# Kernel optimization log

Hardware: AMD Instinct MI355X
Metric: run time of the kernel (lower is better)

## Reference

```python
import jax, jax.numpy as jnp
import numpy as np

N_NODES = 100000
N_EDGES = 1600000
D_IN, D_H, D_OUT = 128, 64, 32


def _linear_init(key, out_dim, in_dim):
    # torch.nn.Linear default init: U(-1/sqrt(in), 1/sqrt(in))
    bound = 1.0 / np.sqrt(in_dim)
    return jax.random.uniform(key, (out_dim, in_dim), jnp.float32, -bound, bound)


def setup_inputs() -> dict:
    key = jax.random.key(0)
    ks = jax.random.split(key, 8)
    x = jax.random.normal(ks[0], (N_NODES, D_IN), dtype=jnp.float32)
    edge_index = jax.random.randint(ks[1], (2, N_EDGES), 0, N_NODES, dtype=jnp.int64)
    return {
        "x": x,
        "edge_index": edge_index,
        # SAGEConv layer 1: lin_l (neighbor agg, with bias), lin_r (root, no bias)
        "W1_l": _linear_init(ks[2], D_H, D_IN),
        "b1": jnp.zeros((D_H,), jnp.float32),
        "W1_r": _linear_init(ks[3], D_H, D_IN),
        # SAGEConv layer 2
        "W2_l": _linear_init(ks[4], D_OUT, D_H),
        "b2": jnp.zeros((D_OUT,), jnp.float32),
        "W2_r": _linear_init(ks[5], D_OUT, D_H),
    }


def _sage_conv(x, src, dst, W_l, b_l, W_r):
    """PyG SAGEConv with mean aggregation: lin_l(mean_{j in N(i)} x_j) + lin_r(x_i)."""
    n = x.shape[0]
    # scatter-mean of source features onto destination nodes
    agg = jax.ops.segment_sum(x[src], dst, num_segments=n)          # [N, d]
    deg = jax.ops.segment_sum(jnp.ones_like(dst, dtype=x.dtype), dst, num_segments=n)
    mean = agg / jnp.maximum(deg, 1.0)[:, None]
    return mean @ W_l.T + b_l + x @ W_r.T


def reference(x, edge_index, W1_l, b1, W1_r, W2_l, b2, W2_r):
    src, dst = edge_index[0], edge_index[1]
    h = _sage_conv(x, src, dst, W1_l, b1, W1_r)
    h = jax.nn.relu(h)
    # dropout p=0.5 is identity in eval mode
    return _sage_conv(h, src, dst, W2_l, b2, W2_r)
```

## Files before the change

kernel.cpp:

```cpp
#include <hip/hip_runtime.h>


namespace {
constexpr int N = 100000;
constexpr int E = 1600000;
constexpr int NBLK = (N + 255) / 256;
constexpr int NT16 = N / 16;
constexpr int NCHUNK = 64;
constexpr int CHUNK_N = 1600;
constexpr int CAP = 28000;
constexpr int PA_BLOCKS = 256;
constexpr int PER_BLK = E / PA_BLOCKS;
}

using bf16x8 = __attribute__((ext_vector_type(8))) short;
using f32x4  = __attribute__((ext_vector_type(4))) float;

__device__ __forceinline__ short f2bf(float f) {
    unsigned u = __builtin_bit_cast(unsigned, f);
    u += 0x7FFFu + ((u >> 16) & 1u);
    return (short)(u >> 16);
}

__device__ __forceinline__ bf16x8 load_frag8(const float* __restrict__ p) {
    const float4* p4 = (const float4*)p;
    float4 f0 = p4[0], f1 = p4[1];
    bf16x8 r;
    r[0] = f2bf(f0.x); r[1] = f2bf(f0.y); r[2] = f2bf(f0.z); r[3] = f2bf(f0.w);
    r[4] = f2bf(f1.x); r[5] = f2bf(f1.y); r[6] = f2bf(f1.z); r[7] = f2bf(f1.w);
    return r;
}

__device__ __forceinline__ float pk_lo(unsigned u) {
    return __builtin_bit_cast(float, u << 16);
}
__device__ __forceinline__ float pk_hi(unsigned u) {
    return __builtin_bit_cast(float, u & 0xFFFF0000u);
}


__global__ __launch_bounds__(256) void detect_dtype(const int* __restrict__ raw,
                                                    int* __restrict__ flag,
                                                    int* __restrict__ bcur) {
    if (threadIdx.x < NCHUNK) bcur[threadIdx.x] = 0;
    int any = 0;
#pragma unroll
    for (int k = 0; k < 64; ++k) {
        int i = threadIdx.x + k * 256;
        any |= raw[2 * i + 1];
    }
    unsigned long long b = __ballot(any != 0);
    __shared__ int acc[4];
    int w = threadIdx.x >> 6;
    if ((threadIdx.x & 63) == 0) acc[w] = (b != 0ULL) ? 1 : 0;
    __syncthreads();
    if (threadIdx.x == 0) *flag = acc[0] | acc[1] | acc[2] | acc[3];
}

__global__ __launch_bounds__(256) void bucket_edges(
        const int* __restrict__ raw, const int* __restrict__ flag,
        int* __restrict__ bcur, int2* __restrict__ bucket) {
    __shared__ int cnt[NCHUNK];
    __shared__ int res[NCHUNK];
    if (threadIdx.x < NCHUNK) cnt[threadIdx.x] = 0;
    __syncthreads();
    const int is32 = *flag;
    const int e0 = blockIdx.x * PER_BLK;
    for (int i = threadIdx.x; i < PER_BLK; i += 256) {
        int e = e0 + i;
        int d = is32 ? raw[E + e] : raw[2 * ((long long)E + e)];
        atomicAdd(&cnt[d / CHUNK_N], 1);
    }
    __syncthreads();
    if (threadIdx.x < NCHUNK) {
        res[threadIdx.x] = atomicAdd(&bcur[threadIdx.x], cnt[threadIdx.x]);
        cnt[threadIdx.x] = 0;
    }
    __syncthreads();
    for (int i = threadIdx.x; i < PER_BLK; i += 256) {
        int e = e0 + i;
        int d, s;
        if (is32) { d = raw[E + e]; s = raw[e]; }
        else      { d = raw[2 * ((long long)E + e)]; s = raw[2 * (long long)e]; }
        int c = d / CHUNK_N;
        int pos = res[c] + atomicAdd(&cnt[c], 1);
        if (pos < CAP) bucket[(size_t)c * CAP + pos] = make_int2(s, d);
    }
}

__global__ __launch_bounds__(1024) void count2(
        const int* __restrict__ bcur, const int2* __restrict__ bucket,
        int* __restrict__ counts) {
    __shared__ int scnt[CHUNK_N];
    const int chunk = blockIdx.x;
    const int lo = chunk * CHUNK_N;
    for (int i = threadIdx.x; i < CHUNK_N; i += 1024) scnt[i] = 0;
    __syncthreads();
    int n = bcur[chunk]; if (n > CAP) n = CAP;
    const int2* b = bucket + (size_t)chunk * CAP;
    for (int i = threadIdx.x; i < n; i += 1024)
        atomicAdd(&scnt[b[i].y - lo], 1);
    __syncthreads();
    const int lim = N - lo;
    for (int i = threadIdx.x; i < CHUNK_N; i += 1024)
        if (i < lim) counts[lo + i] = scnt[i];
}

__global__ __launch_bounds__(256) void scan1(const int* __restrict__ counts,
                                             int* __restrict__ rowstart,
                                             int* __restrict__ bsum) {
    __shared__ int tmp[256];
    int t = threadIdx.x;
    int i = blockIdx.x * 256 + t;
    int v = (i < N) ? counts[i] : 0;
    tmp[t] = v;
    __syncthreads();
#pragma unroll
    for (int off = 1; off < 256; off <<= 1) {
        int a = (t >= off) ? tmp[t - off] : 0;
        __syncthreads();
        tmp[t] += a;
        __syncthreads();
    }
    if (i < N) rowstart[i] = tmp[t] - v;
    if (t == 255) bsum[blockIdx.x] = tmp[255];
}

__global__ __launch_bounds__(512) void scan2(int* __restrict__ bsum) {
    __shared__ int tmp[512];
    int t = threadIdx.x;
    int v = (t < NBLK) ? bsum[t] : 0;
    tmp[t] = v;
    __syncthreads();
#pragma unroll
    for (int off = 1; off < 512; off <<= 1) {
        int a = (t >= off) ? tmp[t - off] : 0;
        __syncthreads();
        tmp[t] += a;
        __syncthreads();
    }
    if (t < NBLK) bsum[t] = tmp[t] - v;
}

__global__ void scan3(int* __restrict__ rowstart, const int* __restrict__ bsum) {
    int i = blockIdx.x * blockDim.x + threadIdx.x;
    if (i < N) rowstart[i] += bsum[i >> 8];
    if (i == 0) rowstart[N] = E;
}

__global__ __launch_bounds__(1024) void fill2(
        const int* __restrict__ bcur, const int2* __restrict__ bucket,
        const int* __restrict__ rowstart, int* __restrict__ csr) {
    __shared__ int scur[CHUNK_N];
    const int chunk = blockIdx.x;
    const int lo = chunk * CHUNK_N;
    const int lim = N - lo;
    for (int i = threadIdx.x; i < CHUNK_N; i += 1024)
        scur[i] = (i < lim) ? rowstart[lo + i] : 0;
    __syncthreads();
    int n = bcur[chunk]; if (n > CAP) n = CAP;
    const int2* b = bucket + (size_t)chunk * CAP;
    for (int i = threadIdx.x; i < n; i += 1024) {
        int2 sd = b[i];
        int pos = atomicAdd(&scur[sd.y - lo], 1);
        csr[pos] = sd.x;
    }
}

__global__ __launch_bounds__(256) void transform1_mfma(
        const float* __restrict__ x, const float* __restrict__ W1l,
        const float* __restrict__ W1r, unsigned short* __restrict__ z1b,
        float* __restrict__ r1) {
    const int lane = threadIdx.x & 63;
    const int gw = blockIdx.x * 4 + (threadIdx.x >> 6);
    const int q = gw & 1;
    const int r16 = lane & 15;
    const int kgrp = lane >> 4;

    bf16x8 wf[2][2][4];
#pragma unroll
    for (int m = 0; m < 2; ++m) {
        const float* W = m ? W1r : W1l;
#pragma unroll
        for (int c = 0; c < 2; ++c) {
            const float* pw = W + (size_t)(q * 32 + c * 16 + r16) * 128 + kgrp * 8;
#pragma unroll
            for (int kb = 0; kb < 4; ++kb)
                wf[m][c][kb] = load_frag8(pw + kb * 32);
        }
    }

    const int stride = (gridDim.x * 4) >> 1;
    for (int t = gw >> 1; t < NT16; t += stride) {
        const float* px = x + ((size_t)t * 16 + r16) * 128 + kgrp * 8;
        bf16x8 af[4];
#pragma unroll
        for (int kb = 0; kb < 4; ++kb) af[kb] = load_frag8(px + kb * 32);

        f32x4 a00 = {0.f,0.f,0.f,0.f}, a01 = {0.f,0.f,0.f,0.f};
        f32x4 a10 = {0.f,0.f,0.f,0.f}, a11 = {0.f,0.f,0.f,0.f};
#pragma unroll
        for (int kb = 0; kb < 4; ++kb) {
            a00 = __builtin_amdgcn_mfma_f32_16x16x32_bf16(af[kb], wf[0][0][kb], a00, 0, 0, 0);
            a01 = __builtin_amdgcn_mfma_f32_16x16x32_bf16(af[kb], wf[0][1][kb], a01, 0, 0, 0);
            a10 = __builtin_amdgcn_mfma_f32_16x16x32_bf16(af[kb], wf[1][0][kb], a10, 0, 0, 0);
            a11 = __builtin_amdgcn_mfma_f32_16x16x32_bf16(af[kb], wf[1][1][kb], a11, 0, 0, 0);
        }
#pragma unroll
        for (int i = 0; i < 4; ++i) {
            size_t row = (size_t)t * 16 + kgrp * 4 + i;
            z1b[row * 64 + q * 32 +  0 + r16] = (unsigned short)f2bf(a00[i]);
            z1b[row * 64 + q * 32 + 16 + r16] = (unsigned short)f2bf(a01[i]);
            r1[row * 64 + q * 32 +  0 + r16] = a10[i];
            r1[row * 64 + q * 32 + 16 + r16] = a11[i];
        }
    }
}

__global__ __launch_bounds__(256) void transform2_mfma(
        const float* __restrict__ h, const float* __restrict__ W2l,
        const float* __restrict__ W2r, unsigned short* __restrict__ z2b,
        float* __restrict__ r2) {
    const int lane = threadIdx.x & 63;
    const int gw = blockIdx.x * 4 + (threadIdx.x >> 6);
    const int r16 = lane & 15;
    const int kgrp = lane >> 4;

    bf16x8 wf[2][2][2];
#pragma unroll
    for (int m = 0; m < 2; ++m) {
        const float* W = m ? W2r : W2l;
#pragma unroll
        for (int c = 0; c < 2; ++c) {
            const float* pw = W + (size_t)(c * 16 + r16) * 64 + kgrp * 8;
#pragma unroll
            for (int kb = 0; kb < 2; ++kb)
                wf[m][c][kb] = load_frag8(pw + kb * 32);
        }
    }

    for (int t = gw; t < NT16; t += gridDim.x * 4) {
        const float* ph = h + ((size_t)t * 16 + r16) * 64 + kgrp * 8;
        bf16x8 af[2];
        af[0] = load_frag8(ph);
        af[1] = load_frag8(ph + 32);

        f32x4 a00 = {0.f,0.f,0.f,0.f}, a01 = {0.f,0.f,0.f,0.f};
        f32x4 a10 = {0.f,0.f,0.f,0.f}, a11 = {0.f,0.f,0.f,0.f};
#pragma unroll
        for (int kb = 0; kb < 2; ++kb) {
            a00 = __builtin_amdgcn_mfma_f32_16x16x32_bf16(af[kb], wf[0][0][kb], a00, 0, 0, 0);
            a01 = __builtin_amdgcn_mfma_f32_16x16x32_bf16(af[kb], wf[0][1][kb], a01, 0, 0, 0);
            a10 = __builtin_amdgcn_mfma_f32_16x16x32_bf16(af[kb], wf[1][0][kb], a10, 0, 0, 0);
            a11 = __builtin_amdgcn_mfma_f32_16x16x32_bf16(af[kb], wf[1][1][kb], a11, 0, 0, 0);
        }
#pragma unroll
        for (int i = 0; i < 4; ++i) {
            size_t row = (size_t)t * 16 + kgrp * 4 + i;
            z2b[row * 32 +  0 + r16] = (unsigned short)f2bf(a00[i]);
            z2b[row * 32 + 16 + r16] = (unsigned short)f2bf(a01[i]);
            r2[row * 32 +  0 + r16] = a10[i];
            r2[row * 32 + 16 + r16] = a11[i];
        }
    }
}


__global__ __launch_bounds__(256) void agg1_fused(
        const int* __restrict__ rowstart, const int* __restrict__ csr,
        const unsigned* __restrict__ z1w, const float* __restrict__ r1,
        const float* __restrict__ b1, float* __restrict__ h) {
    const int n = blockIdx.x * 4 + (threadIdx.x >> 6);
    if (n >= N) return;
    const int lane = threadIdx.x & 63;
    const int half = lane >> 5;
    const int fl = lane & 31;
    const int beg = rowstart[n], end = rowstart[n + 1];
    float alo = 0.f, ahi = 0.f;
    int p = beg;
    for (; p + 8 <= end; p += 8) {
        int c0 = csr[p + 0 + half], c1 = csr[p + 2 + half];
        int c2 = csr[p + 4 + half], c3 = csr[p + 6 + half];
        unsigned u0 = z1w[(size_t)c0 * 32 + fl];
        unsigned u1 = z1w[(size_t)c1 * 32 + fl];
        unsigned u2 = z1w[(size_t)c2 * 32 + fl];
        unsigned u3 = z1w[(size_t)c3 * 32 + fl];
        alo += pk_lo(u0) + pk_lo(u1) + pk_lo(u2) + pk_lo(u3);
        ahi += pk_hi(u0) + pk_hi(u1) + pk_hi(u2) + pk_hi(u3);
    }
    for (; p + 2 <= end; p += 2) {
        int c = csr[p + half];
        unsigned u = z1w[(size_t)c * 32 + fl];
        alo += pk_lo(u);
        ahi += pk_hi(u);
    }
    if (p < end && half == 0) {
        int c = csr[p];
        unsigned u = z1w[(size_t)c * 32 + fl];
        alo += pk_lo(u);
        ahi += pk_hi(u);
    }
    alo += __shfl_xor(alo, 32, 64);
    ahi += __shfl_xor(ahi, 32, 64);
    if (half == 0) {
        float inv = (end > beg) ? 1.0f / (float)(end - beg) : 0.f;
        float2 rv = ((const float2*)r1)[(size_t)n * 32 + fl];
        float2 bv = ((const float2*)b1)[fl];
        float2 o;
        o.x = fmaxf(alo * inv + bv.x + rv.x, 0.f);
        o.y = fmaxf(ahi * inv + bv.y + rv.y, 0.f);
        ((float2*)h)[(size_t)n * 32 + fl] = o;
    }
}

__global__ __launch_bounds__(256) void agg2_fused(
        const int* __restrict__ rowstart, const int* __restrict__ csr,
        const unsigned* __restrict__ z2w, const float* __restrict__ r2,
        const float* __restrict__ b2, float* __restrict__ out) {
    const int n = blockIdx.x * 4 + (threadIdx.x >> 6);
    if (n >= N) return;
    const int lane = threadIdx.x & 63;
    const int quad = lane >> 4;
    const int fl = lane & 15;
    const int beg = rowstart[n], end = rowstart[n + 1];
    float alo = 0.f, ahi = 0.f;
    int p = beg;
    for (; p + 8 <= end; p += 8) {
        int c0 = csr[p + quad], c1 = csr[p + 4 + quad];
        unsigned u0 = z2w[(size_t)c0 * 16 + fl];
        unsigned u1 = z2w[(size_t)c1 * 16 + fl];
        alo += pk_lo(u0) + pk_lo(u1);
        ahi += pk_hi(u0) + pk_hi(u1);
    }
    for (; p + 4 <= end; p += 4) {
        int c = csr[p + quad];
        unsigned u = z2w[(size_t)c * 16 + fl];
        alo += pk_lo(u);
        ahi += pk_hi(u);
    }
    if (p < end) {
        int r = end - p;
        if (quad < r) {
            int c = csr[p + quad];
            unsigned u = z2w[(size_t)c * 16 + fl];
            alo += pk_lo(u);
            ahi += pk_hi(u);
        }
    }
    alo += __shfl_xor(alo, 16, 64);
    ahi += __shfl_xor(ahi, 16, 64);
    alo += __shfl_xor(alo, 32, 64);
    ahi += __shfl_xor(ahi, 32, 64);
    if (lane < 16) {
        float inv = (end > beg) ? 1.0f / (float)(end - beg) : 0.f;
        float2 rv = ((const float2*)r2)[(size_t)n * 16 + fl];
        float2 bv = ((const float2*)b2)[fl];
        float2 o;
        o.x = alo * inv + bv.x + rv.x;
        o.y = ahi * inv + bv.y + rv.y;
        ((float2*)out)[(size_t)n * 16 + fl] = o;
    }
}


extern "C" void kernel_launch(void* const* d_in, const int* in_sizes, int n_in,
                              void* d_out, int out_size, void* d_ws, size_t ws_size,
                              hipStream_t stream) {
    const float* x    = (const float*)d_in[0];
    const int*   raw  = (const int*)d_in[1];
    const float* W1l  = (const float*)d_in[2];
    const float* b1   = (const float*)d_in[3];
    const float* W1r  = (const float*)d_in[4];
    const float* W2l  = (const float*)d_in[5];
    const float* b2   = (const float*)d_in[6];
    const float* W2r  = (const float*)d_in[7];
    float* out = (float*)d_out;

    char* wsb = (char*)d_ws;
    unsigned short* z1b = (unsigned short*)wsb;
    unsigned short* z2b = (unsigned short*)wsb;
    float* r1 = (float*)(wsb + 16 * 1024 * 1024);
    float* r2 = (float*)(wsb + 16 * 1024 * 1024);
    float* h  = (float*)(wsb + 48 * 1024 * 1024);
    int2* bucket = (int2*)(wsb + 48 * 1024 * 1024);

    int* ibase    = (int*)(wsb + 80 * 1024 * 1024);
    int* counts   = ibase;
    int* rowstart = ibase + N;
    int* bsum     = ibase + 2 * N + 1;
    int* csr      = ibase + 2 * N + 1 + 512;
    int* flag     = csr + E;
    int* bcur     = flag + 1;

    detect_dtype<<<1, 256, 0, stream>>>(raw, flag, bcur);
    bucket_edges<<<PA_BLOCKS, 256, 0, stream>>>(raw, flag, bcur, bucket);
    count2<<<NCHUNK, 1024, 0, stream>>>(bcur, bucket, counts);
    scan1<<<NBLK, 256, 0, stream>>>(counts, rowstart, bsum);
    scan2<<<1, 512, 0, stream>>>(bsum);
    scan3<<<NBLK, 256, 0, stream>>>(rowstart, bsum);
    fill2<<<NCHUNK, 1024, 0, stream>>>(bcur, bucket, rowstart, csr);

    transform1_mfma<<<1024, 256, 0, stream>>>(x, W1l, W1r, z1b, r1);
    agg1_fused<<<(N + 3) / 4, 256, 0, stream>>>(rowstart, csr, (const unsigned*)z1b, r1, b1, h);

    transform2_mfma<<<1024, 256, 0, stream>>>(h, W2l, W2r, z2b, r2);
    agg2_fused<<<(N + 3) / 4, 256, 0, stream>>>(rowstart, csr, (const unsigned*)z2b, r2, b2, out);
}
```

Before: 215.7 us.

## Slice layer-1 bf16 features into column panels and aggregate per slice

transform1 now writes the bf16 neighbor features as four column slices of 16 features (32 bytes per node), each stored contiguously for all nodes. The layer-1 aggregation becomes a grid-strided kernel where each block handles one slice and one half of the nodes, so each slice's gather working set (about 3.2 MB) can stay in L2/MALL cache instead of random 128-byte gathers over the full array. The cost is that the CSR is read four times, each gather fetches only 32 bytes, and every wave must do a three-step shuffle reduction. Nontemporal hints are added for the csr, r1 and h streams.

```diff
diff --git a/kernel.cpp b/kernel.cpp
--- a/kernel.cpp
+++ b/kernel.cpp
@@ -209,8 +209,8 @@
 #pragma unroll
         for (int i = 0; i < 4; ++i) {
             size_t row = (size_t)t * 16 + kgrp * 4 + i;
-            z1b[row * 64 + q * 32 +  0 + r16] = (unsigned short)f2bf(a00[i]);
-            z1b[row * 64 + q * 32 + 16 + r16] = (unsigned short)f2bf(a01[i]);
+            z1b[(size_t)(2 * q + 0) * (N * 16) + row * 16 + r16] = (unsigned short)f2bf(a00[i]);
+            z1b[(size_t)(2 * q + 1) * (N * 16) + row * 16 + r16] = (unsigned short)f2bf(a01[i]);
             r1[row * 64 + q * 32 +  0 + r16] = a10[i];
             r1[row * 64 + q * 32 + 16 + r16] = a11[i];
         }
@@ -265,51 +265,57 @@
     }
 }
 
-
-__global__ __launch_bounds__(256) void agg1_fused(
+__global__ __launch_bounds__(256) void agg1_sliced(
         const int* __restrict__ rowstart, const int* __restrict__ csr,
         const unsigned* __restrict__ z1w, const float* __restrict__ r1,
         const float* __restrict__ b1, float* __restrict__ h) {
-    const int n = blockIdx.x * 4 + (threadIdx.x >> 6);
-    if (n >= N) return;
+    const int role = blockIdx.x & 7;
+    const int slice = role >> 1;
+    const int half = role & 1;
     const int lane = threadIdx.x & 63;
-    const int half = lane >> 5;
-    const int fl = lane & 31;
-    const int beg = rowstart[n], end = rowstart[n + 1];
-    float alo = 0.f, ahi = 0.f;
-    int p = beg;
-    for (; p + 8 <= end; p += 8) {
-        int c0 = csr[p + 0 + half], c1 = csr[p + 2 + half];
-        int c2 = csr[p + 4 + half], c3 = csr[p + 6 + half];
-        unsigned u0 = z1w[(size_t)c0 * 32 + fl];
-        unsigned u1 = z1w[(size_t)c1 * 32 + fl];
-        unsigned u2 = z1w[(size_t)c2 * 32 + fl];
-        unsigned u3 = z1w[(size_t)c3 * 32 + fl];
-        alo += pk_lo(u0) + pk_lo(u1) + pk_lo(u2) + pk_lo(u3);
-        ahi += pk_hi(u0) + pk_hi(u1) + pk_hi(u2) + pk_hi(u3);
-    }
-    for (; p + 2 <= end; p += 2) {
-        int c = csr[p + half];
-        unsigned u = z1w[(size_t)c * 32 + fl];
-        alo += pk_lo(u);
-        ahi += pk_hi(u);
-    }
-    if (p < end && half == 0) {
-        int c = csr[p];
-        unsigned u = z1w[(size_t)c * 32 + fl];
-        alo += pk_lo(u);
-        ahi += pk_hi(u);
-    }
-    alo += __shfl_xor(alo, 32, 64);
-    ahi += __shfl_xor(ahi, 32, 64);
-    if (half == 0) {
-        float inv = (end > beg) ? 1.0f / (float)(end - beg) : 0.f;
-        float2 rv = ((const float2*)r1)[(size_t)n * 32 + fl];
-        float2 bv = ((const float2*)b1)[fl];
-        float2 o;
-        o.x = fmaxf(alo * inv + bv.x + rv.x, 0.f);
-        o.y = fmaxf(ahi * inv + bv.y + rv.y, 0.f);
-        ((float2*)h)[(size_t)n * 32 + fl] = o;
+    const int r = lane >> 3, f = lane & 7;
+    const unsigned* zs = z1w + (size_t)slice * (N * 8);
+
+    const int n0 = half * (N / 2);
+    const int n1 = n0 + N / 2;
+    const int wav = (blockIdx.x >> 3) * 4 + (threadIdx.x >> 6);
+    const int nw = (gridDim.x >> 3) * 4;
+
+    float2 bv;
+    {
+        unsigned long long bb = *(const unsigned long long*)(b1 + slice * 16 + 2 * f);
+        bv = __builtin_bit_cast(float2, bb);
+    }
+
+    for (int n = n0 + wav; n < n1; n += nw) {
+        const int beg = rowstart[n], end = rowstart[n + 1];
+        float alo = 0.f, ahi = 0.f;
+        for (int p = beg; p < end; p += 8) {
+            int idx = p + r;
+            if (idx < end) {
+                int c = __builtin_nontemporal_load(&csr[idx]);
+                unsigned u = zs[(size_t)c * 8 + f];
+                alo += pk_lo(u);
+                ahi += pk_hi(u);
+            }
+        }
+        alo += __shfl_xor(alo, 8, 64);
+        ahi += __shfl_xor(ahi, 8, 64);
+        alo += __shfl_xor(alo, 16, 64);
+        ahi += __shfl_xor(ahi, 16, 64);
+        alo += __shfl_xor(alo, 32, 64);
+        ahi += __shfl_xor(ahi, 32, 64);
+        if (lane < 8) {
+            float inv = (end > beg) ? 1.0f / (float)(end - beg) : 0.f;
+            unsigned long long rr = __builtin_nontemporal_load(
+                (const unsigned long long*)(r1 + (size_t)n * 64 + slice * 16 + 2 * f));
+            float2 rv = __builtin_bit_cast(float2, rr);
+            float2 o;
+            o.x = fmaxf(alo * inv + bv.x + rv.x, 0.f);
+            o.y = fmaxf(ahi * inv + bv.y + rv.y, 0.f);
+            __builtin_nontemporal_store(__builtin_bit_cast(unsigned long long, o),
+                (unsigned long long*)(h + (size_t)n * 64 + slice * 16 + 2 * f));
+        }
     }
 }
 
@@ -339,8 +345,8 @@
         ahi += pk_hi(u);
     }
     if (p < end) {
-        int r = end - p;
-        if (quad < r) {
+        int rr = end - p;
+        if (quad < rr) {
             int c = csr[p + quad];
             unsigned u = z2w[(size_t)c * 16 + fl];
             alo += pk_lo(u);
@@ -401,7 +407,7 @@
     fill2<<<NCHUNK, 1024, 0, stream>>>(bcur, bucket, rowstart, csr);
 
     transform1_mfma<<<1024, 256, 0, stream>>>(x, W1l, W1r, z1b, r1);
-    agg1_fused<<<(N + 3) / 4, 256, 0, stream>>>(rowstart, csr, (const unsigned*)z1b, r1, b1, h);
+    agg1_sliced<<<2048, 256, 0, stream>>>(rowstart, csr, (const unsigned*)z1b, r1, b1, h);
 
     transform2_mfma<<<1024, 256, 0, stream>>>(h, W2l, W2r, z2b, r2);
     agg2_fused<<<(N + 3) / 4, 256, 0, stream>>>(rowstart, csr, (const unsigned*)z2b, r2, b2, out);
```

Result: slower. 319.6 us (+48.2%).
